# Performance work log

Measured on AMD Instinct MI355X. Metric: run time of the kernel, lower is better.

Reference implementation:

```python
import jax, jax.numpy as jnp
import numpy as np

LN_EPS = 1e-5


def _gru(x, w_ih, w_hh, b_ih, b_hh):
    # x: [B, T, D_in]; w_ih: [3H, D_in]; w_hh: [3H, H]; PyTorch gate order r, z, n
    B, T, _ = x.shape
    Hd = w_hh.shape[1]
    # Precompute input contributions for all timesteps in one big GEMM
    xg = jnp.einsum('btd,gd->btg', x, w_ih) + b_ih  # [B, T, 3H]

    def step(h, xg_t):
        hg = h @ w_hh.T + b_hh                       # [B, 3H]
        xr, xz, xn = jnp.split(xg_t, 3, axis=-1)
        hr, hz, hn = jnp.split(hg, 3, axis=-1)
        r = jax.nn.sigmoid(xr + hr)
        z = jax.nn.sigmoid(xz + hz)
        n = jnp.tanh(xn + r * hn)
        h_new = (1.0 - z) * n + z * h
        return h_new, h_new

    h0 = jnp.zeros((B, Hd), dtype=x.dtype)
    _, outs = jax.lax.scan(step, h0, jnp.swapaxes(xg, 0, 1))  # [T, B, H]
    return jnp.swapaxes(outs, 0, 1)                           # [B, T, H]


def _layernorm(x, g, b):
    mu = jnp.mean(x, axis=-1, keepdims=True)
    var = jnp.mean(jnp.square(x - mu), axis=-1, keepdims=True)
    return (x - mu) * jax.lax.rsqrt(var + LN_EPS) * g + b


def setup_inputs() -> dict:
    key = jax.random.key(0)
    ks = jax.random.split(key, 10)
    B, T, H = 128, 256, 512
    D_in = 2 * H  # conditional: cat([H, C_embed])
    s_ih = 1.0 / np.sqrt(D_in)
    s_hh = 1.0 / np.sqrt(H)
    return {
        'H': jax.random.normal(ks[0], (B, T, H), jnp.float32),
        'C_embed': jax.random.normal(ks[1], (B, T, H), jnp.float32),
        'w_ih': jax.random.normal(ks[2], (3 * H, D_in), jnp.float32) * s_ih,
        'w_hh': jax.random.normal(ks[3], (3 * H, H), jnp.float32) * s_hh,
        'b_ih': jnp.zeros((3 * H,), jnp.float32),
        'b_hh': jnp.zeros((3 * H,), jnp.float32),
        'fc_mid_w': jax.random.normal(ks[4], (H, H), jnp.float32) * s_hh,
        'fc_mid_b': jnp.zeros((H,), jnp.float32),
        'ln_g': jnp.ones((H,), jnp.float32),
        'ln_b': jnp.zeros((H,), jnp.float32),
        'fc_w': jax.random.normal(ks[5], (1, H), jnp.float32) * s_hh,
        'fc_b': jnp.zeros((1,), jnp.float32),
    }


def reference(H, C_embed, w_ih, w_hh, b_ih, b_hh, fc_mid_w, fc_mid_b, ln_g, ln_b, fc_w, fc_b):
    # conditional critic: concat features along hidden dim
    D_in = jnp.concatenate([H, C_embed], axis=2)           # [B, T, 2H]
    out = _gru(D_in, w_ih, w_hh, b_ih, b_hh)               # [B, T, H]
    # dropout in eval mode -> identity
    out = jnp.einsum('bth,oh->bto', out, fc_mid_w) + fc_mid_b
    out = _layernorm(out, ln_g, ln_b)
    logits = jnp.einsum('bth,oh->bto', out, fc_w) + fc_b   # [B, T, 1]
    return logits
```

## Files before the change

kernel.cpp:

```cpp
#include <hip/hip_runtime.h>
#include <hip/hip_bf16.h>
#include <cstdint>
#include <cstddef>

#define B_   128
#define T_   256
#define TC_  64
#define H_   512
#define G_   1536
#define DIN_ 1024

__global__ __launch_bounds__(256) void k_prep(const float* __restrict__ w_hh,
                                              const float* __restrict__ fc_mid_w,
                                              float4* __restrict__ W4hh,
                                              float4* __restrict__ W4fc)
{
    int tid = blockIdx.x * 256 + threadIdx.x;
    if (tid < 128 * G_) {
        int k4 = tid / G_;
        int r  = tid - k4 * G_;
        const float* s = w_hh + (size_t)r * H_ + k4 * 4;
        W4hh[tid] = make_float4(s[0], s[1], s[2], s[3]);
    }
    if (tid < 128 * H_) {
        int k4 = tid / H_;
        int c  = tid - k4 * H_;
        const float* s = fc_mid_w + (size_t)c * H_ + k4 * 4;
        W4fc[tid] = make_float4(s[0], s[1], s[2], s[3]);
    }
}

__global__ __launch_bounds__(256) void k_xg(const float* __restrict__ Hin,
                                            const float* __restrict__ Ce,
                                            const float* __restrict__ w_ih,
                                            const float* __restrict__ b_ih,
                                            float* __restrict__ xgc,
                                            const int c0)
{
    __shared__ float As[16][132];
    __shared__ float Bs[16][132];
    const int tid = threadIdx.x;
    const int n0 = blockIdx.x * 128;
    const int m0 = blockIdx.y * 128;
    const int tx = tid & 15;
    const int ty = tid >> 4;
    const int lr = tid >> 2;
    const int lk = (tid & 3) * 4;

    float acc[8][8];
    #pragma unroll
    for (int i = 0; i < 8; ++i)
        #pragma unroll
        for (int j = 0; j < 8; ++j) acc[i][j] = 0.f;

    for (int k0 = 0; k0 < DIN_; k0 += 16) {
        const bool first = (k0 < 512);
        #pragma unroll
        for (int h = 0; h < 2; ++h) {
            int mr   = lr + h * 64;
            int mr_g = m0 + mr;
            int b    = mr_g >> 6;
            int tc   = mr_g & 63;
            size_t row = (size_t)b * T_ + c0 + tc;
            const float* src = first ? (Hin + row * 512 + (k0 + lk))
                                     : (Ce  + row * 512 + (k0 - 512 + lk));
            float4 v = *reinterpret_cast<const float4*>(src);
            As[lk + 0][mr] = v.x;
            As[lk + 1][mr] = v.y;
            As[lk + 2][mr] = v.z;
            As[lk + 3][mr] = v.w;
        }
        #pragma unroll
        for (int h = 0; h < 2; ++h) {
            int nr = lr + h * 64;
            const float* src = w_ih + (size_t)(n0 + nr) * DIN_ + k0 + lk;
            float4 v = *reinterpret_cast<const float4*>(src);
            Bs[lk + 0][nr] = v.x;
            Bs[lk + 1][nr] = v.y;
            Bs[lk + 2][nr] = v.z;
            Bs[lk + 3][nr] = v.w;
        }
        __syncthreads();
        #pragma unroll
        for (int kk = 0; kk < 16; ++kk) {
            float a[8], b[8];
            *reinterpret_cast<float4*>(&a[0]) = *reinterpret_cast<const float4*>(&As[kk][ty * 8]);
            *reinterpret_cast<float4*>(&a[4]) = *reinterpret_cast<const float4*>(&As[kk][ty * 8 + 4]);
            *reinterpret_cast<float4*>(&b[0]) = *reinterpret_cast<const float4*>(&Bs[kk][tx * 8]);
            *reinterpret_cast<float4*>(&b[4]) = *reinterpret_cast<const float4*>(&Bs[kk][tx * 8 + 4]);
            #pragma unroll
            for (int i = 0; i < 8; ++i)
                #pragma unroll
                for (int j = 0; j < 8; ++j)
                    acc[i][j] = fmaf(a[i], b[j], acc[i][j]);
        }
        __syncthreads();
    }

    float4 bv0 = *reinterpret_cast<const float4*>(b_ih + n0 + tx * 8);
    float4 bv1 = *reinterpret_cast<const float4*>(b_ih + n0 + tx * 8 + 4);
    #pragma unroll
    for (int i = 0; i < 8; ++i) {
        size_t m = (size_t)(m0 + ty * 8 + i);
        float* dst = xgc + m * G_ + n0 + tx * 8;
        *reinterpret_cast<float4*>(dst) =
            make_float4(acc[i][0] + bv0.x, acc[i][1] + bv0.y, acc[i][2] + bv0.z, acc[i][3] + bv0.w);
        *reinterpret_cast<float4*>(dst + 4) =
            make_float4(acc[i][4] + bv1.x, acc[i][5] + bv1.y, acc[i][6] + bv1.z, acc[i][7] + bv1.w);
    }
}

__global__ __launch_bounds__(256) void k_step(const float4* __restrict__ W4hh,
                                              const float* __restrict__ b_hh,
                                              const float* __restrict__ xgc,
                                              float* __restrict__ h_all,
                                              const int t)
{
    __shared__ float hs[16][520];
    const int tid = threadIdx.x;
    const int j0 = blockIdx.x * 16;
    const int b0 = blockIdx.y * 16;

    if (t > 0) {
        #pragma unroll
        for (int i = 0; i < 8; ++i) {
            int idx = i * 256 + tid;
            int bl = idx >> 7;
            int p  = (idx & 127) * 4;
            float4 v = *reinterpret_cast<const float4*>(
                h_all + ((size_t)(b0 + bl) * T_ + (t - 1)) * H_ + p);
            *reinterpret_cast<float4*>(&hs[bl][p]) = v;
        }
    } else {
        #pragma unroll
        for (int i = 0; i < 8; ++i) {
            int idx = i * 256 + tid;
            int bl = idx >> 7;
            int p  = (idx & 127) * 4;
            *reinterpret_cast<float4*>(&hs[bl][p]) = make_float4(0.f, 0.f, 0.f, 0.f);
        }
    }
    __syncthreads();

    const int jl = tid & 15;
    const int bl = tid >> 4;
    const int j  = j0 + jl;

    float ar = 0.f, az = 0.f, an = 0.f;
    const float4* wp = W4hh + j;
    const float* hrow = hs[bl];
    #pragma unroll 4
    for (int k4 = 0; k4 < 128; ++k4) {
        float4 h4 = *reinterpret_cast<const float4*>(hrow + k4 * 4);
        float4 w0 = wp[(size_t)k4 * G_];
        float4 w1 = wp[(size_t)k4 * G_ + 512];
        float4 w2 = wp[(size_t)k4 * G_ + 1024];
        ar = fmaf(w0.x, h4.x, fmaf(w0.y, h4.y, fmaf(w0.z, h4.z, fmaf(w0.w, h4.w, ar))));
        az = fmaf(w1.x, h4.x, fmaf(w1.y, h4.y, fmaf(w1.z, h4.z, fmaf(w1.w, h4.w, az))));
        an = fmaf(w2.x, h4.x, fmaf(w2.y, h4.y, fmaf(w2.z, h4.z, fmaf(w2.w, h4.w, an))));
    }

    float hr = ar + b_hh[j];
    float hz = az + b_hh[512 + j];
    float hn = an + b_hh[1024 + j];
    size_t mx = (size_t)(b0 + bl) * TC_ + (t & 63);
    const float* xgm = xgc + mx * G_;
    float xr = xgm[j], xz = xgm[512 + j], xn = xgm[1024 + j];
    float r = 1.f / (1.f + expf(-(xr + hr)));
    float z = 1.f / (1.f + expf(-(xz + hz)));
    float n = tanhf(xn + r * hn);
    float hp = hrow[j];
    h_all[((size_t)(b0 + bl) * T_ + t) * H_ + j] = (1.f - z) * n + z * hp;
}

__global__ __launch_bounds__(256) void k_head(const float* __restrict__ h_all,
                                              const float4* __restrict__ W4fc,
                                              const float* __restrict__ fc_mid_b,
                                              const float* __restrict__ ln_g,
                                              const float* __restrict__ ln_b,
                                              const float* __restrict__ fc_w,
                                              const float* __restrict__ fc_b,
                                              float* __restrict__ out)
{
    __shared__ float hsm[16][520];
    const int tid = threadIdx.x;
    const size_t r0 = (size_t)blockIdx.x * 16;

    #pragma unroll
    for (int i = 0; i < 8; ++i) {
        int idx = i * 256 + tid;
        int rl = idx >> 7;
        int p  = (idx & 127) * 4;
        *reinterpret_cast<float4*>(&hsm[rl][p]) =
            *reinterpret_cast<const float4*>(h_all + (r0 + rl) * H_ + p);
    }
    __syncthreads();

    float accA[16], accB[16];
    #pragma unroll
    for (int i = 0; i < 16; ++i) { accA[i] = 0.f; accB[i] = 0.f; }
    const int cA = tid, cB = tid + 256;
    for (int k4 = 0; k4 < 128; ++k4) {
        float4 wA = W4fc[k4 * 512 + cA];
        float4 wB = W4fc[k4 * 512 + cB];
        #pragma unroll
        for (int rr = 0; rr < 16; ++rr) {
            float4 h4 = *reinterpret_cast<const float4*>(&hsm[rr][k4 * 4]);
            accA[rr] = fmaf(wA.x, h4.x, fmaf(wA.y, h4.y, fmaf(wA.z, h4.z, fmaf(wA.w, h4.w, accA[rr]))));
            accB[rr] = fmaf(wB.x, h4.x, fmaf(wB.y, h4.y, fmaf(wB.z, h4.z, fmaf(wB.w, h4.w, accB[rr]))));
        }
    }
    __syncthreads();
    const float bA = fc_mid_b[cA], bB = fc_mid_b[cB];
    #pragma unroll
    for (int rr = 0; rr < 16; ++rr) {
        hsm[rr][cA] = accA[rr] + bA;
        hsm[rr][cB] = accB[rr] + bB;
    }
    __syncthreads();

    const int lane = tid & 63;
    const int wv   = tid >> 6;
    float gw[8];
    float sgw = 0.f, sbw = 0.f;
    #pragma unroll
    for (int i = 0; i < 8; ++i) {
        int c = lane + i * 64;
        float g = ln_g[c], w = fc_w[c];
        gw[i] = g * w;
        sgw += gw[i];
        sbw += ln_b[c] * w;
    }
    #pragma unroll
    for (int off = 32; off; off >>= 1) {
        sgw += __shfl_xor(sgw, off);
        sbw += __shfl_xor(sbw, off);
    }
    const float fcb0 = fc_b[0];
    for (int rr = wv; rr < 16; rr += 4) {
        float s1 = 0.f, s2 = 0.f, sg = 0.f;
        #pragma unroll
        for (int i = 0; i < 8; ++i) {
            float y = hsm[rr][lane + i * 64];
            s1 += y; s2 += y * y; sg += gw[i] * y;
        }
        #pragma unroll
        for (int off = 32; off; off >>= 1) {
            s1 += __shfl_xor(s1, off);
            s2 += __shfl_xor(s2, off);
            sg += __shfl_xor(sg, off);
        }
        if (lane == 0) {
            float mu   = s1 * (1.f / 512.f);
            float var  = s2 * (1.f / 512.f) - mu * mu;
            float rstd = rsqrtf(var + 1e-5f);
            out[r0 + rr] = rstd * (sg - mu * sgw) + sbw + fcb0;
        }
    }
}

extern "C" void kernel_launch(void* const* d_in, const int* in_sizes, int n_in,
                              void* d_out, int out_size, void* d_ws, size_t ws_size,
                              hipStream_t stream)
{
    const float* Hin  = (const float*)d_in[0];
    const float* Ce   = (const float*)d_in[1];
    const float* w_ih = (const float*)d_in[2];
    const float* w_hh = (const float*)d_in[3];
    const float* b_ih = (const float*)d_in[4];
    const float* b_hh = (const float*)d_in[5];
    const float* fcmw = (const float*)d_in[6];
    const float* fcmb = (const float*)d_in[7];
    const float* lng  = (const float*)d_in[8];
    const float* lnb  = (const float*)d_in[9];
    const float* fcw  = (const float*)d_in[10];
    const float* fcb  = (const float*)d_in[11];
    float* out = (float*)d_out;

    float* ws     = (float*)d_ws;
    float* xgc    = ws;
    float* hall   = xgc + (size_t)B_ * TC_ * G_;
    float* w4hh_f = hall + (size_t)B_ * T_ * H_;
    float* w4fc_f = w4hh_f + (size_t)128 * G_ * 4;
    float4* W4hh  = (float4*)w4hh_f;
    float4* W4fc  = (float4*)w4fc_f;

    hipLaunchKernelGGL(k_prep, dim3(768), dim3(256), 0, stream, w_hh, fcmw, W4hh, W4fc);
    for (int c = 0; c < T_ / TC_; ++c) {
        hipLaunchKernelGGL(k_xg, dim3(12, 64), dim3(256), 0, stream,
                           Hin, Ce, w_ih, b_ih, xgc, c * TC_);
        for (int tc = 0; tc < TC_; ++tc)
            hipLaunchKernelGGL(k_step, dim3(32, 8), dim3(256), 0, stream,
                               W4hh, b_hh, xgc, hall, c * TC_ + tc);
    }
    hipLaunchKernelGGL(k_head, dim3(2048), dim3(256), 0, stream,
                       hall, W4fc, fcmb, lng, lnb, fcw, fcb, out);
}
```

Measured before the change: 5.702 ms.

## Fuse GRU timesteps into persistent kernel with LDS-resident weights and grid barrier

Replaces the 64 per-timestep k_step launches in each chunk with a single persistent k_scan64 kernel. Each block loads its 16-column slice of the recurrent weights into LDS once and then loops over the chunk's timesteps. Blocks synchronise between steps through a global atomic counter barrier instead of kernel boundaries. This removes per-step launch overhead and repeated global reads of W_hh. In exchange it needs about 128KB of dynamic LDS per block, and all 256 blocks must be co-resident or the spin barrier deadlocks.

New measurement: 11.28 ms. 97.8% more time.

```diff
diff --git a/kernel.cpp b/kernel.cpp
--- a/kernel.cpp
+++ b/kernel.cpp
@@ -9,6 +9,7 @@
 #define H_   512
 #define G_   1536
 #define DIN_ 1024
+#define NBLK_ 256
 
 __global__ __launch_bounds__(256) void k_prep(const float* __restrict__ w_hh,
                                               const float* __restrict__ fc_mid_w,
@@ -110,67 +111,88 @@
     }
 }
 
-__global__ __launch_bounds__(256) void k_step(const float4* __restrict__ W4hh,
-                                              const float* __restrict__ b_hh,
-                                              const float* __restrict__ xgc,
-                                              float* __restrict__ h_all,
-                                              const int t)
-{
-    __shared__ float hs[16][520];
+__global__ __launch_bounds__(256) void k_scan64(const float4* __restrict__ W4hh,
+                                                const float* __restrict__ b_hh,
+                                                const float* __restrict__ xgc,
+                                                float* __restrict__ h_all,
+                                                unsigned int* __restrict__ cnt,
+                                                const int c0)
+{
+    extern __shared__ float4 smem4[];
+    float4* Wl = smem4;
+    float4* hs = smem4 + 6144;
+
     const int tid = threadIdx.x;
-    const int j0 = blockIdx.x * 16;
-    const int b0 = blockIdx.y * 16;
-
-    if (t > 0) {
-        #pragma unroll
-        for (int i = 0; i < 8; ++i) {
-            int idx = i * 256 + tid;
-            int bl = idx >> 7;
-            int p  = (idx & 127) * 4;
-            float4 v = *reinterpret_cast<const float4*>(
-                h_all + ((size_t)(b0 + bl) * T_ + (t - 1)) * H_ + p);
-            *reinterpret_cast<float4*>(&hs[bl][p]) = v;
-        }
-    } else {
-        #pragma unroll
-        for (int i = 0; i < 8; ++i) {
-            int idx = i * 256 + tid;
-            int bl = idx >> 7;
-            int p  = (idx & 127) * 4;
-            *reinterpret_cast<float4*>(&hs[bl][p]) = make_float4(0.f, 0.f, 0.f, 0.f);
-        }
-    }
-    __syncthreads();
-
-    const int jl = tid & 15;
-    const int bl = tid >> 4;
-    const int j  = j0 + jl;
-
-    float ar = 0.f, az = 0.f, an = 0.f;
-    const float4* wp = W4hh + j;
-    const float* hrow = hs[bl];
-    #pragma unroll 4
-    for (int k4 = 0; k4 < 128; ++k4) {
-        float4 h4 = *reinterpret_cast<const float4*>(hrow + k4 * 4);
-        float4 w0 = wp[(size_t)k4 * G_];
-        float4 w1 = wp[(size_t)k4 * G_ + 512];
-        float4 w2 = wp[(size_t)k4 * G_ + 1024];
-        ar = fmaf(w0.x, h4.x, fmaf(w0.y, h4.y, fmaf(w0.z, h4.z, fmaf(w0.w, h4.w, ar))));
-        az = fmaf(w1.x, h4.x, fmaf(w1.y, h4.y, fmaf(w1.z, h4.z, fmaf(w1.w, h4.w, az))));
-        an = fmaf(w2.x, h4.x, fmaf(w2.y, h4.y, fmaf(w2.z, h4.z, fmaf(w2.w, h4.w, an))));
-    }
-
-    float hr = ar + b_hh[j];
-    float hz = az + b_hh[512 + j];
-    float hn = an + b_hh[1024 + j];
-    size_t mx = (size_t)(b0 + bl) * TC_ + (t & 63);
-    const float* xgm = xgc + mx * G_;
-    float xr = xgm[j], xz = xgm[512 + j], xn = xgm[1024 + j];
-    float r = 1.f / (1.f + expf(-(xr + hr)));
-    float z = 1.f / (1.f + expf(-(xz + hz)));
-    float n = tanhf(xn + r * hn);
-    float hp = hrow[j];
-    h_all[((size_t)(b0 + bl) * T_ + t) * H_ + j] = (1.f - z) * n + z * hp;
+    const int jl  = tid & 15;
+    const int bl  = tid >> 4;
+    const int j0  = blockIdx.x * 16;
+    const int b0  = blockIdx.y * 16;
+    const int j   = j0 + jl;
+
+    for (int i = tid; i < 6144; i += 256) {
+        int k4 = i / 48;
+        int r  = i - k4 * 48;
+        int g  = r >> 4;
+        int jj = r & 15;
+        Wl[i] = W4hh[(size_t)k4 * G_ + g * 512 + j0 + jj];
+    }
+    const float bhr = b_hh[j];
+    const float bhz = b_hh[512 + j];
+    const float bhn = b_hh[1024 + j];
+
+    for (int s = 0; s < TC_; ++s) {
+        const int t = c0 + s;
+        if (t > 0) {
+            for (int i = tid; i < 2048; i += 256) {
+                int row = i >> 7, k4 = i & 127;
+                hs[row * 130 + k4] = *reinterpret_cast<const float4*>(
+                    h_all + ((size_t)(b0 + row) * T_ + (t - 1)) * H_ + k4 * 4);
+            }
+        } else {
+            for (int i = tid; i < 2048; i += 256) {
+                int row = i >> 7, k4 = i & 127;
+                hs[row * 130 + k4] = make_float4(0.f, 0.f, 0.f, 0.f);
+            }
+        }
+        __syncthreads();
+
+        float ar = 0.f, az = 0.f, an = 0.f;
+        const float4* hrow = hs + (size_t)bl * 130;
+        const float4* wp   = Wl + jl;
+        #pragma unroll 4
+        for (int k4 = 0; k4 < 128; ++k4) {
+            float4 h4 = hrow[k4];
+            float4 w0 = wp[(k4 * 3 + 0) * 16];
+            float4 w1 = wp[(k4 * 3 + 1) * 16];
+            float4 w2 = wp[(k4 * 3 + 2) * 16];
+            ar = fmaf(w0.x, h4.x, fmaf(w0.y, h4.y, fmaf(w0.z, h4.z, fmaf(w0.w, h4.w, ar))));
+            az = fmaf(w1.x, h4.x, fmaf(w1.y, h4.y, fmaf(w1.z, h4.z, fmaf(w1.w, h4.w, az))));
+            an = fmaf(w2.x, h4.x, fmaf(w2.y, h4.y, fmaf(w2.z, h4.z, fmaf(w2.w, h4.w, an))));
+        }
+
+        float hr = ar + bhr;
+        float hz = az + bhz;
+        float hn = an + bhn;
+        const float* xgm = xgc + ((size_t)(b0 + bl) * TC_ + s) * G_;
+        float xr = xgm[j], xz = xgm[512 + j], xn = xgm[1024 + j];
+        float r = 1.f / (1.f + expf(-(xr + hr)));
+        float z = 1.f / (1.f + expf(-(xz + hz)));
+        float n = tanhf(xn + r * hn);
+        float hp = reinterpret_cast<const float*>(hrow)[j & 511];
+        h_all[((size_t)(b0 + bl) * T_ + t) * H_ + j] = (1.f - z) * n + z * hp;
+
+        if (s < TC_ - 1) {
+            __threadfence();
+            __syncthreads();
+            if (tid == 0) {
+                __hip_atomic_fetch_add(cnt, 1u, __ATOMIC_RELEASE, __HIP_MEMORY_SCOPE_AGENT);
+                const unsigned int target = (unsigned int)NBLK_ * (unsigned int)(s + 1);
+                while (__hip_atomic_load(cnt, __ATOMIC_ACQUIRE, __HIP_MEMORY_SCOPE_AGENT) < target)
+                    __builtin_amdgcn_s_sleep(2);
+            }
+            __syncthreads();
+        }
+    }
 }
 
 __global__ __launch_bounds__(256) void k_head(const float* __restrict__ h_all,
@@ -282,16 +304,18 @@
     float* hall   = xgc + (size_t)B_ * TC_ * G_;
     float* w4hh_f = hall + (size_t)B_ * T_ * H_;
     float* w4fc_f = w4hh_f + (size_t)128 * G_ * 4;
+    unsigned int* cnt = (unsigned int*)(w4fc_f + (size_t)128 * H_ * 4);
     float4* W4hh  = (float4*)w4hh_f;
     float4* W4fc  = (float4*)w4fc_f;
 
+    hipMemsetAsync(cnt, 0, 4 * sizeof(unsigned int), stream);
     hipLaunchKernelGGL(k_prep, dim3(768), dim3(256), 0, stream, w_hh, fcmw, W4hh, W4fc);
     for (int c = 0; c < T_ / TC_; ++c) {
         hipLaunchKernelGGL(k_xg, dim3(12, 64), dim3(256), 0, stream,
                            Hin, Ce, w_ih, b_ih, xgc, c * TC_);
-        for (int tc = 0; tc < TC_; ++tc)
-            hipLaunchKernelGGL(k_step, dim3(32, 8), dim3(256), 0, stream,
-                               W4hh, b_hh, xgc, hall, c * TC_ + tc);
+        hipLaunchKernelGGL(k_scan64, dim3(32, 8), dim3(256),
+                           (6144 + 2080) * sizeof(float4), stream,
+                           W4hh, b_hh, xgc, hall, cnt + c, c * TC_);
     }
     hipLaunchKernelGGL(k_head, dim3(2048), dim3(256), 0, stream,
                        hall, W4fc, fcmb, lng, lnb, fcw, fcb, out);
```
